# Kernel tuning notes

Measured on AMD Instinct MI355X. Metric: run time of the kernel, lower is better.

Reference implementation:

```python
import jax, jax.numpy as jnp
import numpy as np

N_NODES = 50000
DIM = 128
NEG_SLOPE = 0.2


def _gat_conv(x, W, a_src, a_dst, b, src, dst, n):
    # PyG GATConv, single head, self-loops already appended to (src, dst).
    h = x @ W.T                              # [N, D]
    asrc = h @ a_src                         # [N]
    adst = h @ a_dst                         # [N]
    e = jax.nn.leaky_relu(asrc[src] + adst[dst], NEG_SLOPE)  # [E]
    emax = jax.ops.segment_max(e, dst, num_segments=n)
    emax = jnp.where(jnp.isfinite(emax), emax, 0.0)
    ex = jnp.exp(e - emax[dst])
    denom = jax.ops.segment_sum(ex, dst, num_segments=n)
    coef = ex / (denom[dst] + 1e-16)         # segment softmax over incoming edges
    out = jax.ops.segment_sum(coef[:, None] * h[src], dst, num_segments=n)
    return out + b


def _l2norm(x):
    # F.normalize(x) row-wise, eps=1e-12
    n = jnp.sqrt(jnp.sum(x * x, axis=1, keepdims=True))
    return x / jnp.maximum(n, 1e-12)


def setup_inputs() -> dict:
    key = jax.random.key(0)
    ks = jax.random.split(key, 24)
    d = DIM
    inp = {
        'entity_feat_1': jax.random.normal(ks[0], (N_NODES, d), jnp.float32),
        'image_feat': jax.random.normal(ks[1], (N_NODES, 4096), jnp.float32),
        'text_feat': jax.random.normal(ks[2], (N_NODES, 768), jnp.float32),
        'graph_edges': jax.random.randint(ks[3], (2, 600000), 0, N_NODES, jnp.int64),
        'entity_feat': jax.random.normal(ks[4], (N_NODES, d), jnp.float32) * (6.0 / (N_NODES + d)) ** 0.5 * 100,
        'W_img': jax.random.normal(ks[5], (d, 4096), jnp.float32) * 0.02,
        'b_img': jnp.zeros((d,), jnp.float32),
        'W_txt': jax.random.normal(ks[6], (d, 768), jnp.float32) * 0.03,
        'b_txt': jnp.zeros((d,), jnp.float32),
        'W_fus': jax.random.normal(ks[7], (d, 3 * d), jnp.float32) * 0.05,
        'b_fus': jnp.zeros((d,), jnp.float32),
    }
    for i, tag in enumerate(['e', 'i', 't']):
        base = 8 + 4 * i
        inp['W%s_gat' % tag] = jax.random.normal(ks[base], (d, d), jnp.float32) * 0.08
        inp['a%s_src' % tag] = jax.random.normal(ks[base + 1], (d,), jnp.float32) * 0.1
        inp['a%s_dst' % tag] = jax.random.normal(ks[base + 2], (d,), jnp.float32) * 0.1
        inp['b%s_gat' % tag] = jnp.zeros((d,), jnp.float32)
    return inp


def reference(entity_feat_1, image_feat, text_feat, graph_edges, entity_feat,
              W_img, b_img, W_txt, b_txt, W_fus, b_fus,
              We_gat, ae_src, ae_dst, be_gat,
              Wi_gat, ai_src, ai_dst, bi_gat,
              Wt_gat, at_src, at_dst, bt_gat):
    n = entity_feat.shape[0]
    loops = jnp.arange(n, dtype=graph_edges.dtype)
    src = jnp.concatenate([graph_edges[0], loops])
    dst = jnp.concatenate([graph_edges[1], loops])
    img = image_feat @ W_img.T + b_img
    txt = text_feat @ W_txt.T + b_txt
    # GraphConv = GATConv -> dropout(eval: identity) -> F.normalize
    e_out = _l2norm(_gat_conv(entity_feat, We_gat, ae_src, ae_dst, be_gat, src, dst, n))
    i_out = _l2norm(_gat_conv(img, Wi_gat, ai_src, ai_dst, bi_gat, src, dst, n))
    t_out = _l2norm(_gat_conv(txt, Wt_gat, at_src, at_dst, bt_gat, src, dst, n))
    mm = jnp.concatenate([e_out, i_out, t_out], axis=1) @ W_fus.T + b_fus
    return (e_out, i_out, t_out, mm)
```

## Files before the change

kernel.cpp:

```cpp
#include <hip/hip_runtime.h>
#include <hip/hip_bf16.h>

typedef __attribute__((ext_vector_type(8))) short bf16x8;
typedef __attribute__((ext_vector_type(4))) short bf16x4;
typedef __attribute__((ext_vector_type(4))) float f32x4;

#define LDS_A2 16384
#define LDS_HALF2 32768

__device__ __forceinline__ float fin(float v) {
    return (v == v && v > -1e30f && v < 1e30f) ? v : 0.f;
}
__device__ __forceinline__ float lrelu(float v) {
    return (v >= 0.f) ? v : 0.2f * v;
}
__device__ __forceinline__ unsigned f2bu(float f) {
    unsigned u = __builtin_bit_cast(unsigned, f);
    return (u + 0x7FFFu + ((u >> 16) & 1u)) >> 16;
}
__device__ __forceinline__ short f2b(float f) { return (short)f2bu(f); }
__device__ __forceinline__ float bflo(unsigned u) {
    return __builtin_bit_cast(float, u << 16);
}
__device__ __forceinline__ float bfhi(unsigned u) {
    return __builtin_bit_cast(float, u & 0xffff0000u);
}

template<int FUSE, int AD, int HP, int NT>
__device__ __forceinline__
void gemm_body(const float* __restrict__ A0, const float* __restrict__ A1,
               const float* __restrict__ A2,
               const __hip_bfloat16* __restrict__ Bw,
               const float* __restrict__ bias,
               const float* __restrict__ av1, const float* __restrict__ av2,
               float* __restrict__ asrc, float* __restrict__ adst, int astride,
               float* __restrict__ Cf, unsigned* __restrict__ Cp, int cpstride,
               int M, int K, int bx)
{
    __shared__ __align__(16) char smem[2][LDS_HALF2];
    const int tid = threadIdx.x;
    const int l  = tid & 63;
    const int lr = l & 15;
    const int lk = l >> 4;
    const int w  = tid >> 6;
    const int brow = bx * 128;
    const int nt = K >> 6;

    f32x4 acc[8];
#pragma unroll
    for (int j = 0; j < 8; j++) acc[j] = (f32x4){0.f, 0.f, 0.f, 0.f};

    f32x4 va[4];
    bf16x8 vb16[2];

    auto stage_load = [&](int t) {
        const int k0 = t << 6;
#pragma unroll
        for (int i = 0; i < 4; i++) {
            int elem = (i * 512 + tid) * 4;
            int row = elem >> 6;
            int col = elem & 63;
            int gr = brow + row; if (gr >= M) gr = M - 1;
            int gcol = k0 + col;
            const float* p;
            if (FUSE) {
                int seg = gcol >> 7;
                const float* s = (seg == 0) ? A0 : (seg == 1) ? A1 : A2;
                p = s + (size_t)gr * 128 + (gcol & 127);
            } else {
                p = A0 + (size_t)gr * (size_t)K + gcol;
            }
            va[i] = NT ? __builtin_nontemporal_load((const f32x4*)p)
                       : *(const f32x4*)p;
        }
#pragma unroll
        for (int i = 0; i < 2; i++) {
            int elem = (i * 512 + tid) * 8;
            int row = elem >> 6;
            int col = elem & 63;
            vb16[i] = *(const bf16x8*)(Bw + (size_t)row * (size_t)K + k0 + col);
        }
    };
    auto stage_write = [&](int buf) {
#pragma unroll
        for (int i = 0; i < 4; i++) {
            int elem = (i * 512 + tid) * 4;
            int row = elem >> 6;
            int col = elem & 63;
            int slo = (col * 2) ^ ((row & 7) << 4);
            bf16x4 a4 = {f2b(va[i].x), f2b(va[i].y), f2b(va[i].z), f2b(va[i].w)};
            *(bf16x4*)(&smem[buf][row * 128 + slo]) = a4;
        }
#pragma unroll
        for (int i = 0; i < 2; i++) {
            int elem = (i * 512 + tid) * 8;
            int row = elem >> 6;
            int col = elem & 63;
            int slo = (col * 2) ^ ((row & 7) << 4);
            *(bf16x8*)(&smem[buf][LDS_A2 + row * 128 + slo]) = vb16[i];
        }
    };

    stage_load(0);
    stage_write(0);
    __syncthreads();
    int cur = 0;
    for (int t = 0; t < nt; t++) {
        if (t + 1 < nt) stage_load(t + 1);
        const char* Ab = &smem[cur][0];
        const char* Bb = &smem[cur][LDS_A2];
#pragma unroll
        for (int ks = 0; ks < 2; ks++) {
            bf16x8 af, bv[8];
            {
                int row = w * 16 + lr;
                int lo  = (ks * 64 + lk * 16) ^ ((row & 7) << 4);
                af = *(const bf16x8*)(Ab + row * 128 + lo);
            }
#pragma unroll
            for (int nf = 0; nf < 8; nf++) {
                int row = nf * 16 + lr;
                int lo  = (ks * 64 + lk * 16) ^ ((row & 7) << 4);
                bv[nf] = *(const bf16x8*)(Bb + row * 128 + lo);
            }
#pragma unroll
            for (int nf = 0; nf < 8; nf++)
                acc[nf] = __builtin_amdgcn_mfma_f32_16x16x32_bf16(
                    af, bv[nf], acc[nf], 0, 0, 0);
        }
        if (t + 1 < nt) stage_write(cur ^ 1);
        __syncthreads();
        cur ^= 1;
    }

#pragma unroll
    for (int j = 0; j < 4; j++) {
        int row = brow + w * 16 + lk * 4 + j;
        float vv[8];
        float s1 = 0.f, s2 = 0.f;
#pragma unroll
        for (int nf = 0; nf < 8; nf++) {
            int col = nf * 16 + lr;
            float v = acc[nf][j];
            if (bias) v += bias[col];
            v = fin(v);
            vv[nf] = v;
            if (AD) { s1 += v * av1[col]; s2 += v * av2[col]; }
            if (!HP && row < M) Cf[(size_t)row * 128 + col] = v;
        }
        if (HP && row < M) {
#pragma unroll
            for (int nf = 0; nf < 4; nf++) {
                int col = nf * 16 + lr;
                Cp[(size_t)row * cpstride + col] = f2bu(vv[nf]) | (f2bu(vv[nf + 4]) << 16);
            }
        }
        if (AD) {
#pragma unroll
            for (int o = 1; o < 16; o <<= 1) {
                s1 += __shfl_xor(s1, o);
                s2 += __shfl_xor(s2, o);
            }
            if (lr == 0 && row < M) {
                asrc[(size_t)row * astride] = fin(s1);
                adst[(size_t)row * astride] = fin(s2);
            }
        }
    }
}

__global__ __launch_bounds__(512, 4)
void hgemm3b(const float* __restrict__ x0, const float* __restrict__ x1,
             const float* __restrict__ x2,
             const __hip_bfloat16* __restrict__ w0,
             const __hip_bfloat16* __restrict__ w1,
             const __hip_bfloat16* __restrict__ w2,
             const float* __restrict__ bc1, const float* __restrict__ bc2,
             const float* __restrict__ a10, const float* __restrict__ a11,
             const float* __restrict__ a12,
             const float* __restrict__ a20, const float* __restrict__ a21,
             const float* __restrict__ a22,
             unsigned* __restrict__ hpAll,
             float* __restrict__ asrc4, float* __restrict__ adst4,
             int M, int K0, int K1, int K2)
{
    int g = blockIdx.y;
    const float* x  = (g == 0) ? x0 : (g == 1) ? x1 : x2;
    const __hip_bfloat16* wv = (g == 0) ? w0 : (g == 1) ? w1 : w2;
    const float* bias = (g == 0) ? nullptr : (g == 1) ? bc1 : bc2;
    const float* av1 = (g == 0) ? a10 : (g == 1) ? a11 : a12;
    const float* av2 = (g == 0) ? a20 : (g == 1) ? a21 : a22;
    int K = (g == 0) ? K0 : (g == 1) ? K1 : K2;
    gemm_body<0, 1, 1, 1>(x, nullptr, nullptr, wv, bias, av1, av2,
                          asrc4 + g, adst4 + g, 4,
                          nullptr, hpAll + g * 64, 192, M, K, blockIdx.x);
}

__global__ __launch_bounds__(512, 4)
void gemm_fus(const float* __restrict__ A0, const float* __restrict__ A1,
              const float* __restrict__ A2, const __hip_bfloat16* __restrict__ Bw,
              const float* __restrict__ bias, float* __restrict__ Cf, int M)
{
    gemm_body<1, 0, 0, 0>(A0, A1, A2, Bw, bias, nullptr, nullptr,
                          nullptr, nullptr, 1, Cf, nullptr, 1, M, 384, blockIdx.x);
}

__global__ __launch_bounds__(256)
void k_compose(const float* __restrict__ Wg1, const float* __restrict__ Wb1,
               const float* __restrict__ bb1, __hip_bfloat16* __restrict__ Wc1,
               float* __restrict__ bc1, int K1,
               const float* __restrict__ Wg2, const float* __restrict__ Wb2,
               const float* __restrict__ bb2, __hip_bfloat16* __restrict__ Wc2,
               float* __restrict__ bc2, int K2)
{
    int y = blockIdx.y;
    const float* Wg  = y ? Wg2 : Wg1;
    const float* Wb  = y ? Wb2 : Wb1;
    const float* bb  = y ? bb2 : bb1;
    __hip_bfloat16* Wc = y ? Wc2 : Wc1;
    float* bc = y ? bc2 : bc1;
    int Kbig = y ? K2 : K1;
    int tid = threadIdx.x;

    if (blockIdx.x == gridDim.x - 1) {
        __shared__ float bs[128];
        if (tid < 128) bs[tid] = bb[tid];
        __syncthreads();
        if (tid < 128) {
            float s = 0.f;
            for (int m = 0; m < 128; m++) s = fmaf(Wg[tid * 128 + m], bs[m], s);
            bc[tid] = fin(s);
        }
        return;
    }
    __shared__ float WgL[128 * 128];
    for (int i = tid; i < 128 * 128; i += 256) WgL[i] = Wg[i];
    __syncthreads();
    int j = blockIdx.x * 64 + (tid & 63);
    if (j >= Kbig) return;
    int g = tid >> 6;
    float acc[32];
#pragma unroll
    for (int i = 0; i < 32; i++) acc[i] = 0.f;
    for (int k = 0; k < 128; k++) {
        float wvv = Wb[(size_t)k * Kbig + j];
#pragma unroll
        for (int i = 0; i < 32; i++)
            acc[i] = fmaf(WgL[(g * 32 + i) * 128 + k], wvv, acc[i]);
    }
#pragma unroll
    for (int i = 0; i < 32; i++)
        *((short*)Wc + (size_t)(g * 32 + i) * Kbig + j) = f2b(acc[i]);
}

__global__ void k_cvt2(const float* __restrict__ s0, const float* __restrict__ s1,
                       __hip_bfloat16* __restrict__ d0, __hip_bfloat16* __restrict__ d1,
                       int n0, int n1)
{
    int g = blockIdx.y;
    const float* s = g ? s1 : s0;
    __hip_bfloat16* d = g ? d1 : d0;
    int n = g ? n1 : n0;
    for (int i = blockIdx.x * blockDim.x + threadIdx.x; i * 4 < n;
         i += gridDim.x * blockDim.x) {
        f32x4 v = *(const f32x4*)(s + (size_t)i * 4);
        bf16x4 b = {f2b(v.x), f2b(v.y), f2b(v.z), f2b(v.w)};
        *(bf16x4*)((short*)d + (size_t)i * 4) = b;
    }
}

__global__ void k_init(const int* __restrict__ e, int* __restrict__ flag,
                       int* __restrict__ deg, int* __restrict__ cursor, int n)
{
    if (blockIdx.x == 0 && threadIdx.x < 64) {
        int v = e[2 * threadIdx.x + 1];
        unsigned long long b = __ballot(v != 0);
        if (threadIdx.x == 0) flag[0] = (b == 0ull) ? 1 : 0;
    }
    for (int i = blockIdx.x * blockDim.x + threadIdx.x; i < n;
         i += gridDim.x * blockDim.x) {
        deg[i] = 0;
        cursor[i] = 0;
    }
}

__global__ void k_degree(const int* __restrict__ e, const int* __restrict__ flag,
                         int* __restrict__ deg, int e0, int n)
{
    int i = blockIdx.x * blockDim.x + threadIdx.x;
    if (i >= e0 + n) return;
    int d;
    if (i < e0) d = flag[0] ? e[2 * e0 + 2 * i] : e[e0 + i];
    else        d = i - e0;
    if ((unsigned)d >= (unsigned)n) d = 0;
    atomicAdd(&deg[d], 1);
}

__global__ void k_scan1(const int* __restrict__ deg, int* __restrict__ csum, int n)
{
    __shared__ int sh[512];
    int c = blockIdx.x, t = threadIdx.x, i = c * 512 + t;
    sh[t] = (i < n) ? deg[i] : 0;
    __syncthreads();
    for (int o = 256; o; o >>= 1) {
        if (t < o) sh[t] += sh[t + o];
        __syncthreads();
    }
    if (t == 0) csum[c] = sh[0];
}

__global__ void k_scan2(const int* __restrict__ csum, int* __restrict__ coff,
                        int nc, int* __restrict__ indptr, int n, int total)
{
    __shared__ int sh[128];
    int t = threadIdx.x;
    int v = (t < nc) ? csum[t] : 0;
    sh[t] = v;
    __syncthreads();
    for (int o = 1; o < 128; o <<= 1) {
        int add = (t >= o) ? sh[t - o] : 0;
        __syncthreads();
        sh[t] += add;
        __syncthreads();
    }
    if (t < nc) coff[t] = sh[t] - v;
    if (t == 0) indptr[n] = total;
}

__global__ void k_scan3(const int* __restrict__ deg, const int* __restrict__ coff,
                        int* __restrict__ indptr, int n)
{
    __shared__ int sh[512];
    int c = blockIdx.x, t = threadIdx.x, i = c * 512 + t;
    int v = (i < n) ? deg[i] : 0;
    sh[t] = v;
    __syncthreads();
    for (int o = 1; o < 512; o <<= 1) {
        int add = (t >= o) ? sh[t - o] : 0;
        __syncthreads();
        sh[t] += add;
        __syncthreads();
    }
    if (i < n) indptr[i] = coff[c] + sh[t] - v;
}

__global__ void k_scatter(const int* __restrict__ e, const int* __restrict__ flag,
                          const int* __restrict__ indptr,
                          int* __restrict__ cursor, int* __restrict__ csr,
                          int e0, int n)
{
    int i = blockIdx.x * blockDim.x + threadIdx.x;
    if (i >= e0 + n) return;
    int s, d;
    if (i < e0) {
        if (flag[0]) { s = e[2 * i]; d = e[2 * e0 + 2 * i]; }
        else         { s = e[i];     d = e[e0 + i]; }
    } else {
        s = d = i - e0;
    }
    if ((unsigned)d >= (unsigned)n) d = 0;
    if ((unsigned)s >= (unsigned)n) s = 0;
    int pos = atomicAdd(&cursor[d], 1);
    csr[indptr[d] + pos] = s;
}

__global__ __launch_bounds__(256)
void gat3(const int* __restrict__ indptr, const int* __restrict__ csr,
          const unsigned* __restrict__ hpAll,
          const float* __restrict__ asrc4, const float* __restrict__ adst4,
          const float* __restrict__ bE, const float* __restrict__ bI,
          const float* __restrict__ bT,
          float* __restrict__ oE, float* __restrict__ oI, float* __restrict__ oT,
          int n)
{
    int node = blockIdx.x * 4 + (threadIdx.x >> 6);
    if (node >= n) return;
    int l = threadIdx.x & 63;
    int beg = indptr[node], end = indptr[node + 1];
    int deg_n = end - beg;
    float adE = adst4[(size_t)node * 4 + 0];
    float adI = adst4[(size_t)node * 4 + 1];
    float adT = adst4[(size_t)node * 4 + 2];
    float aE0 = 0.f, aE1 = 0.f, aI0 = 0.f, aI1 = 0.f, aT0 = 0.f, aT1 = 0.f;

    if (deg_n <= 64) {
        int t = beg + l;
        bool valid = t < end;
        int sidx = valid ? csr[t] : 0;
        if ((unsigned)sidx >= (unsigned)n) sidx = 0;
        float eE = -1e30f, eI = -1e30f, eT = -1e30f;
        if (valid) {
            const float* ap = asrc4 + (size_t)sidx * 4;
            eE = lrelu(ap[0] + adE);
            eI = lrelu(ap[1] + adI);
            eT = lrelu(ap[2] + adT);
        }
        float mE = eE, mI = eI, mT = eT;
        for (int o = 32; o; o >>= 1) {
            mE = fmaxf(mE, __shfl_xor(mE, o));
            mI = fmaxf(mI, __shfl_xor(mI, o));
            mT = fmaxf(mT, __shfl_xor(mT, o));
        }
        float xE = valid ? __expf(eE - mE) : 0.f;
        float xI = valid ? __expf(eI - mI) : 0.f;
        float xT = valid ? __expf(eT - mT) : 0.f;
        float sE = xE, sI = xI, sT = xT;
        for (int o = 32; o; o >>= 1) {
            sE += __shfl_xor(sE, o);
            sI += __shfl_xor(sI, o);
            sT += __shfl_xor(sT, o);
        }
        float iE = 1.f / (sE + 1e-16f);
        float iI = 1.f / (sI + 1e-16f);
        float iT = 1.f / (sT + 1e-16f);
        for (int j = 0; j < deg_n; j++) {
            int   sj = __shfl(sidx, j);
            float cE = __shfl(xE, j) * iE;
            float cI = __shfl(xI, j) * iI;
            float cT = __shfl(xT, j) * iT;
            const unsigned* hb = hpAll + (size_t)sj * 192;
            unsigned uE = hb[l];
            unsigned uI = hb[64 + l];
            unsigned uT = hb[128 + l];
            aE0 += cE * bflo(uE); aE1 += cE * bfhi(uE);
            aI0 += cI * bflo(uI); aI1 += cI * bfhi(uI);
            aT0 += cT * bflo(uT); aT1 += cT * bfhi(uT);
        }
    } else {
        float ad3[3] = {adE, adI, adT};
        float* acc0[3] = {&aE0, &aI0, &aT0};
        float* acc1[3] = {&aE1, &aI1, &aT1};
        for (int g = 0; g < 3; g++) {
            float m = -1e30f;
            for (int t = beg + l; t < end; t += 64) {
                int sidx = csr[t];
                if ((unsigned)sidx >= (unsigned)n) sidx = 0;
                m = fmaxf(m, lrelu(asrc4[(size_t)sidx * 4 + g] + ad3[g]));
            }
            for (int o = 32; o; o >>= 1) m = fmaxf(m, __shfl_xor(m, o));
            float s = 0.f;
            for (int t = beg + l; t < end; t += 64) {
                int sidx = csr[t];
                if ((unsigned)sidx >= (unsigned)n) sidx = 0;
                s += __expf(lrelu(asrc4[(size_t)sidx * 4 + g] + ad3[g]) - m);
            }
            for (int o = 32; o; o >>= 1) s += __shfl_xor(s, o);
            float inv = 1.f / (s + 1e-16f);
            for (int t = beg; t < end; t++) {
                int sidx = csr[t];
                if ((unsigned)sidx >= (unsigned)n) sidx = 0;
                float c = __expf(lrelu(asrc4[(size_t)sidx * 4 + g] + ad3[g]) - m) * inv;
                unsigned u = hpAll[(size_t)sidx * 192 + g * 64 + l];
                *acc0[g] += c * bflo(u);
                *acc1[g] += c * bfhi(u);
            }
        }
    }

    {
        float a0 = aE0 + bE[l], a1 = aE1 + bE[64 + l];
        float ss = a0 * a0 + a1 * a1;
        for (int o = 32; o; o >>= 1) ss += __shfl_xor(ss, o);
        float r = 1.f / fmaxf(sqrtf(fin(ss)), 1e-12f);
        oE[(size_t)node * 128 + l]      = fin(a0 * r);
        oE[(size_t)node * 128 + 64 + l] = fin(a1 * r);
    }
    {
        float a0 = aI0 + bI[l], a1 = aI1 + bI[64 + l];
        float ss = a0 * a0 + a1 * a1;
        for (int o = 32; o; o >>= 1) ss += __shfl_xor(ss, o);
        float r = 1.f / fmaxf(sqrtf(fin(ss)), 1e-12f);
        oI[(size_t)node * 128 + l]      = fin(a0 * r);
        oI[(size_t)node * 128 + 64 + l] = fin(a1 * r);
    }
    {
        float a0 = aT0 + bT[l], a1 = aT1 + bT[64 + l];
        float ss = a0 * a0 + a1 * a1;
        for (int o = 32; o; o >>= 1) ss += __shfl_xor(ss, o);
        float r = 1.f / fmaxf(sqrtf(fin(ss)), 1e-12f);
        oT[(size_t)node * 128 + l]      = fin(a0 * r);
        oT[(size_t)node * 128 + 64 + l] = fin(a1 * r);
    }
}

extern "C" void kernel_launch(void* const* d_in, const int* in_sizes, int n_in,
                              void* d_out, int out_size, void* d_ws, size_t ws_size,
                              hipStream_t stream)
{
    int s0 = n_in - 22;
    if (s0 < 0 || s0 > 1)
        s0 = (in_sizes[1] > in_sizes[0]) ? 1 : 0;

    const float* image_feat  = (const float*)d_in[s0 + 0];
    const float* text_feat   = (const float*)d_in[s0 + 1];
    const int*   edges       = (const int*)d_in[s0 + 2];
    const float* entity_feat = (const float*)d_in[s0 + 3];
    const float* W_img = (const float*)d_in[s0 + 4];
    const float* b_img = (const float*)d_in[s0 + 5];
    const float* W_txt = (const float*)d_in[s0 + 6];
    const float* b_txt = (const float*)d_in[s0 + 7];
    const float* W_fus = (const float*)d_in[s0 + 8];
    const float* b_fus = (const float*)d_in[s0 + 9];
    const float* Wg[3]  = {(const float*)d_in[s0 + 10], (const float*)d_in[s0 + 14],
                           (const float*)d_in[s0 + 18]};
    const float* Avv[3] = {(const float*)d_in[s0 + 11], (const float*)d_in[s0 + 15],
                           (const float*)d_in[s0 + 19]};
    const float* Dvv[3] = {(const float*)d_in[s0 + 12], (const float*)d_in[s0 + 16],
                           (const float*)d_in[s0 + 20]};
    const float* Bg[3]  = {(const float*)d_in[s0 + 13], (const float*)d_in[s0 + 17],
                           (const float*)d_in[s0 + 21]};

    const int n  = in_sizes[s0 + 3] / 128;
    int e0 = in_sizes[s0 + 2] / 2;
    if (e0 == 24 * n) e0 = 12 * n;
    const int ne = e0 + n;
    const int Kimg = in_sizes[s0 + 4] / 128;
    const int Ktxt = in_sizes[s0 + 6] / 128;

    char* ws = (char*)d_ws;
    size_t off = 0;
    auto alloc = [&](size_t b) { size_t o = off; off = (off + b + 255) & ~(size_t)255; return o; };
    int* eflag  = (int*)(ws + alloc(256));
    int* deg    = (int*)(ws + alloc((size_t)n * 4));
    int* indptr = (int*)(ws + alloc((size_t)(n + 1) * 4));
    int* cursor = (int*)(ws + alloc((size_t)n * 4));
    int* csum   = (int*)(ws + alloc(512));
    int* coff   = (int*)(ws + alloc(512));
    float* asrc4 = (float*)(ws + alloc((size_t)n * 16));
    float* adst4 = (float*)(ws + alloc((size_t)n * 16));
    int* csr    = (int*)(ws + alloc((size_t)ne * 4));
    __hip_bfloat16* Wgb0  = (__hip_bfloat16*)(ws + alloc(128 * 128 * 2));
    __hip_bfloat16* Wfusb = (__hip_bfloat16*)(ws + alloc(384 * 128 * 2));
    __hip_bfloat16* Wcimg = (__hip_bfloat16*)(ws + alloc((size_t)Kimg * 128 * 2));
    __hip_bfloat16* Wctxt = (__hip_bfloat16*)(ws + alloc((size_t)Ktxt * 128 * 2));
    float* bcimg = (float*)(ws + alloc(512));
    float* bctxt = (float*)(ws + alloc(512));
    unsigned* hpAll = (unsigned*)(ws + alloc((size_t)n * 192 * 4));
    (void)ws_size; (void)out_size;

    float* out = (float*)d_out;
    float* oE = out;
    float* oI = out + (size_t)n * 128;
    float* oT = out + 2 * (size_t)n * 128;
    float* oM = out + 3 * (size_t)n * 128;

    k_init<<<208, 256, 0, stream>>>(edges, eflag, deg, cursor, n);
    k_cvt2<<<dim3(64, 2), 256, 0, stream>>>(Wg[0], W_fus, Wgb0, Wfusb,
                                            128 * 128, 384 * 128);
    k_compose<<<dim3(Kimg / 64 + 1, 2), 256, 0, stream>>>(
        Wg[1], W_img, b_img, Wcimg, bcimg, Kimg,
        Wg[2], W_txt, b_txt, Wctxt, bctxt, Ktxt);
    k_degree<<<(ne + 255) / 256, 256, 0, stream>>>(edges, eflag, deg, e0, n);
    const int nch = (n + 511) / 512;
    k_scan1<<<nch, 512, 0, stream>>>(deg, csum, n);
    k_scan2<<<1, 128, 0, stream>>>(csum, coff, nch, indptr, n, ne);
    k_scan3<<<nch, 512, 0, stream>>>(deg, coff, indptr, n);
    k_scatter<<<(ne + 255) / 256, 256, 0, stream>>>(edges, eflag, indptr, cursor, csr, e0, n);

    const int mb = (n + 127) / 128;
    hgemm3b<<<dim3(mb, 3), 512, 0, stream>>>(entity_feat, image_feat, text_feat,
                                             Wgb0, Wcimg, Wctxt, bcimg, bctxt,
                                             Avv[0], Avv[1], Avv[2],
                                             Dvv[0], Dvv[1], Dvv[2],
                                             hpAll, asrc4, adst4,
                                             n, 128, Kimg, Ktxt);

    gat3<<<(n + 3) / 4, 256, 0, stream>>>(indptr, csr, hpAll,
                                          asrc4, adst4, Bg[0], Bg[1], Bg[2],
                                          oE, oI, oT, n);

    gemm_fus<<<mb, 512, 0, stream>>>(oE, oI, oT, Wfusb, b_fus, oM, n);
}
```

Before: 452.6 us.

## Pre-swizzle bf16 weights and stream them directly into LDS via global_load_lds

Weight matrices are now stored in global memory already XOR-swizzled to the LDS layout, written that way by the conversion and compose kernels. The GEMM then copies the B tile straight from global memory into LDS with global_load_lds, which removes the per-stage register staging and the separate LDS writes. The compose kernel also moves to 512 threads with 16 accumulators per thread instead of 256 threads with 32. The risk is a synchronization hazard: the async LDS load of the next stage writes the other buffer, and whether that completes before the barrier depends on the code that is not shown.

```diff
diff --git a/kernel.cpp b/kernel.cpp
--- a/kernel.cpp
+++ b/kernel.cpp
@@ -24,13 +24,16 @@
 }
 __device__ __forceinline__ float bfhi(unsigned u) {
     return __builtin_bit_cast(float, u & 0xffff0000u);
+}
+__device__ __forceinline__ size_t swzidx(int r, int j, int K) {
+    return (size_t)r * K + (j & ~63) + ((j & 63) ^ ((r & 7) << 3));
 }
 
 template<int FUSE, int AD, int HP, int NT>
 __device__ __forceinline__
 void gemm_body(const float* __restrict__ A0, const float* __restrict__ A1,
                const float* __restrict__ A2,
-               const __hip_bfloat16* __restrict__ Bw,
+               const short* __restrict__ Bw,
                const float* __restrict__ bias,
                const float* __restrict__ av1, const float* __restrict__ av2,
                float* __restrict__ asrc, float* __restrict__ adst, int astride,
@@ -51,9 +54,8 @@
     for (int j = 0; j < 8; j++) acc[j] = (f32x4){0.f, 0.f, 0.f, 0.f};
 
     f32x4 va[4];
-    bf16x8 vb16[2];
-
-    auto stage_load = [&](int t) {
+
+    auto stage_load = [&](int t, int buf) {
         const int k0 = t << 6;
 #pragma unroll
         for (int i = 0; i < 4; i++) {
@@ -75,10 +77,14 @@
         }
 #pragma unroll
         for (int i = 0; i < 2; i++) {
-            int elem = (i * 512 + tid) * 8;
-            int row = elem >> 6;
-            int col = elem & 63;
-            vb16[i] = *(const bf16x8*)(Bw + (size_t)row * (size_t)K + k0 + col);
+            int L   = (i * 512 + tid) * 16;
+            int row = L >> 7;
+            int slo = L & 127;
+            const short* gp = Bw + (size_t)row * K + t * 64 + (slo >> 1);
+            __builtin_amdgcn_global_load_lds(
+                (const __attribute__((address_space(1))) void*)gp,
+                (__attribute__((address_space(3))) void*)&smem[buf][LDS_A2 + L],
+                16, 0, 0);
         }
     };
     auto stage_write = [&](int buf) {
@@ -91,22 +97,14 @@
             bf16x4 a4 = {f2b(va[i].x), f2b(va[i].y), f2b(va[i].z), f2b(va[i].w)};
             *(bf16x4*)(&smem[buf][row * 128 + slo]) = a4;
         }
-#pragma unroll
-        for (int i = 0; i < 2; i++) {
-            int elem = (i * 512 + tid) * 8;
-            int row = elem >> 6;
-            int col = elem & 63;
-            int slo = (col * 2) ^ ((row & 7) << 4);
-            *(bf16x8*)(&smem[buf][LDS_A2 + row * 128 + slo]) = vb16[i];
-        }
     };
 
-    stage_load(0);
+    stage_load(0, 0);
     stage_write(0);
     __syncthreads();
     int cur = 0;
     for (int t = 0; t < nt; t++) {
-        if (t + 1 < nt) stage_load(t + 1);
+        if (t + 1 < nt) stage_load(t + 1, cur ^ 1);
         const char* Ab = &smem[cur][0];
         const char* Bb = &smem[cur][LDS_A2];
 #pragma unroll
@@ -172,9 +170,8 @@
 __global__ __launch_bounds__(512, 4)
 void hgemm3b(const float* __restrict__ x0, const float* __restrict__ x1,
              const float* __restrict__ x2,
-             const __hip_bfloat16* __restrict__ w0,
-             const __hip_bfloat16* __restrict__ w1,
-             const __hip_bfloat16* __restrict__ w2,
+             const short* __restrict__ w0, const short* __restrict__ w1,
+             const short* __restrict__ w2,
              const float* __restrict__ bc1, const float* __restrict__ bc2,
              const float* __restrict__ a10, const float* __restrict__ a11,
              const float* __restrict__ a12,
@@ -186,7 +183,7 @@
 {
     int g = blockIdx.y;
     const float* x  = (g == 0) ? x0 : (g == 1) ? x1 : x2;
-    const __hip_bfloat16* wv = (g == 0) ? w0 : (g == 1) ? w1 : w2;
+    const short* wv = (g == 0) ? w0 : (g == 1) ? w1 : w2;
     const float* bias = (g == 0) ? nullptr : (g == 1) ? bc1 : bc2;
     const float* av1 = (g == 0) ? a10 : (g == 1) ? a11 : a12;
     const float* av2 = (g == 0) ? a20 : (g == 1) ? a21 : a22;
@@ -198,26 +195,26 @@
 
 __global__ __launch_bounds__(512, 4)
 void gemm_fus(const float* __restrict__ A0, const float* __restrict__ A1,
-              const float* __restrict__ A2, const __hip_bfloat16* __restrict__ Bw,
+              const float* __restrict__ A2, const short* __restrict__ Bw,
               const float* __restrict__ bias, float* __restrict__ Cf, int M)
 {
     gemm_body<1, 0, 0, 0>(A0, A1, A2, Bw, bias, nullptr, nullptr,
                           nullptr, nullptr, 1, Cf, nullptr, 1, M, 384, blockIdx.x);
 }
 
-__global__ __launch_bounds__(256)
+__global__ __launch_bounds__(512)
 void k_compose(const float* __restrict__ Wg1, const float* __restrict__ Wb1,
-               const float* __restrict__ bb1, __hip_bfloat16* __restrict__ Wc1,
+               const float* __restrict__ bb1, short* __restrict__ Wc1,
                float* __restrict__ bc1, int K1,
                const float* __restrict__ Wg2, const float* __restrict__ Wb2,
-               const float* __restrict__ bb2, __hip_bfloat16* __restrict__ Wc2,
+               const float* __restrict__ bb2, short* __restrict__ Wc2,
                float* __restrict__ bc2, int K2)
 {
     int y = blockIdx.y;
     const float* Wg  = y ? Wg2 : Wg1;
     const float* Wb  = y ? Wb2 : Wb1;
     const float* bb  = y ? bb2 : bb1;
-    __hip_bfloat16* Wc = y ? Wc2 : Wc1;
+    short* Wc = y ? Wc2 : Wc1;
     float* bc = y ? bc2 : bc1;
     int Kbig = y ? K2 : K1;
     int tid = threadIdx.x;
@@ -234,38 +231,44 @@
         return;
     }
     __shared__ float WgL[128 * 128];
-    for (int i = tid; i < 128 * 128; i += 256) WgL[i] = Wg[i];
+    for (int i = tid; i < 128 * 128; i += 512) WgL[i] = Wg[i];
     __syncthreads();
     int j = blockIdx.x * 64 + (tid & 63);
     if (j >= Kbig) return;
     int g = tid >> 6;
-    float acc[32];
-#pragma unroll
-    for (int i = 0; i < 32; i++) acc[i] = 0.f;
+    float acc[16];
+#pragma unroll
+    for (int i = 0; i < 16; i++) acc[i] = 0.f;
     for (int k = 0; k < 128; k++) {
         float wvv = Wb[(size_t)k * Kbig + j];
 #pragma unroll
-        for (int i = 0; i < 32; i++)
-            acc[i] = fmaf(WgL[(g * 32 + i) * 128 + k], wvv, acc[i]);
-    }
-#pragma unroll
-    for (int i = 0; i < 32; i++)
-        *((short*)Wc + (size_t)(g * 32 + i) * Kbig + j) = f2b(acc[i]);
+        for (int i = 0; i < 16; i++)
+            acc[i] = fmaf(WgL[(g * 16 + i) * 128 + k], wvv, acc[i]);
+    }
+#pragma unroll
+    for (int i = 0; i < 16; i++) {
+        int r = g * 16 + i;
+        Wc[swzidx(r, j, Kbig)] = f2b(acc[i]);
+    }
 }
 
 __global__ void k_cvt2(const float* __restrict__ s0, const float* __restrict__ s1,
-                       __hip_bfloat16* __restrict__ d0, __hip_bfloat16* __restrict__ d1,
-                       int n0, int n1)
+                       short* __restrict__ d0, short* __restrict__ d1,
+                       int n0, int n1, int K0, int K1)
 {
     int g = blockIdx.y;
     const float* s = g ? s1 : s0;
-    __hip_bfloat16* d = g ? d1 : d0;
+    short* d = g ? d1 : d0;
     int n = g ? n1 : n0;
+    int K = g ? K1 : K0;
     for (int i = blockIdx.x * blockDim.x + threadIdx.x; i * 4 < n;
          i += gridDim.x * blockDim.x) {
-        f32x4 v = *(const f32x4*)(s + (size_t)i * 4);
+        int e = i * 4;
+        int r = e / K;
+        int j = e - r * K;
+        f32x4 v = *(const f32x4*)(s + (size_t)e);
         bf16x4 b = {f2b(v.x), f2b(v.y), f2b(v.z), f2b(v.w)};
-        *(bf16x4*)((short*)d + (size_t)i * 4) = b;
+        *(bf16x4*)(d + swzidx(r, j, K)) = b;
     }
 }
 
@@ -529,10 +532,10 @@
     float* asrc4 = (float*)(ws + alloc((size_t)n * 16));
     float* adst4 = (float*)(ws + alloc((size_t)n * 16));
     int* csr    = (int*)(ws + alloc((size_t)ne * 4));
-    __hip_bfloat16* Wgb0  = (__hip_bfloat16*)(ws + alloc(128 * 128 * 2));
-    __hip_bfloat16* Wfusb = (__hip_bfloat16*)(ws + alloc(384 * 128 * 2));
-    __hip_bfloat16* Wcimg = (__hip_bfloat16*)(ws + alloc((size_t)Kimg * 128 * 2));
-    __hip_bfloat16* Wctxt = (__hip_bfloat16*)(ws + alloc((size_t)Ktxt * 128 * 2));
+    short* Wgb0  = (short*)(ws + alloc(128 * 128 * 2));
+    short* Wfusb = (short*)(ws + alloc(384 * 128 * 2));
+    short* Wcimg = (short*)(ws + alloc((size_t)Kimg * 128 * 2));
+    short* Wctxt = (short*)(ws + alloc((size_t)Ktxt * 128 * 2));
     float* bcimg = (float*)(ws + alloc(512));
     float* bctxt = (float*)(ws + alloc(512));
     unsigned* hpAll = (unsigned*)(ws + alloc((size_t)n * 192 * 4));
@@ -546,8 +549,8 @@
 
     k_init<<<208, 256, 0, stream>>>(edges, eflag, deg, cursor, n);
     k_cvt2<<<dim3(64, 2), 256, 0, stream>>>(Wg[0], W_fus, Wgb0, Wfusb,
-                                            128 * 128, 384 * 128);
-    k_compose<<<dim3(Kimg / 64 + 1, 2), 256, 0, stream>>>(
+                                            128 * 128, 384 * 128, 128, 384);
+    k_compose<<<dim3(Kimg / 64 + 1, 2), 512, 0, stream>>>(
         Wg[1], W_img, b_img, Wcimg, bcimg, Kimg,
         Wg[2], W_txt, b_txt, Wctxt, bctxt, Ktxt);
     k_degree<<<(ne + 255) / 256, 256, 0, stream>>>(edges, eflag, deg, e0, n);
```

After: 448.3 us. Within noise of the previous version (-0.9%).
